# Kernel tuning notes

Hardware: AMD Instinct MI355X
Metric: run time of the kernel (lower is better)

## Reference

```python
import jax, jax.numpy as jnp
import numpy as np

K, D, N = 32, 64, 65536
LOG_2PI = float(np.log(2.0 * np.pi))


def setup_inputs() -> dict:
    key = jax.random.key(0)
    k1, k2, k3, k4 = jax.random.split(key, 4)
    X = jax.random.normal(k1, (N, D), dtype=jnp.float32)
    loc = jax.random.normal(k2, (K, D), dtype=jnp.float32)
    # SPD full covariances per component: A A^T + I
    A = 0.1 * jax.random.normal(k3, (K, D, D), dtype=jnp.float32)
    cov = jnp.einsum('kij,klj->kil', A, A) + jnp.eye(D, dtype=jnp.float32)
    pi = jax.random.normal(k4, (K,), dtype=jnp.float32)
    return {"X": X, "loc": loc, "cov": cov, "pi": pi}


def _gmm_log_prob(X, loc, cov, pi):
    d = X.shape[-1]
    L = jnp.linalg.cholesky(cov)                       # [K, d, d]
    diff = X[:, None, :] - loc[None, :, :]             # [N, K, d]
    # per-component triangular solve: z_k = L_k^{-1} (x - mu_k)
    solve = lambda Lk, dk: jax.scipy.linalg.solve_triangular(Lk, dk.T, lower=True)  # [d, N]
    z = jax.vmap(solve, in_axes=(0, 1))(L, diff)       # [K, d, N]
    maha = jnp.sum(z * z, axis=1).T                    # [N, K]
    half_logdet = jnp.sum(jnp.log(jnp.diagonal(L, axis1=-2, axis2=-1)), axis=-1)  # [K]
    comp_logp = -0.5 * (d * LOG_2PI + maha) - half_logdet[None, :]  # [N, K]
    # Categorical(softmax(pi)).logits followed by log_softmax == log_softmax(pi)
    weighted = comp_logp + jax.nn.log_softmax(pi)[None, :]
    return jax.scipy.special.logsumexp(weighted, axis=1, keepdims=True)  # [N, 1]


def reference(X, loc, cov, pi):
    return _gmm_log_prob(X, loc, cov, pi)
```

## Files before the change

kernel.cpp:

```cpp
#include <hip/hip_runtime.h>
#include <math.h>

#define KCOMP 32
#define DDIM 64
#define LOG_2PI 1.8378770664093453f

#define WFRAG_HALF8S 64
#define WCOMP_BYTES 10240

typedef _Float16 half8 __attribute__((ext_vector_type(8)));
typedef float floatx16 __attribute__((ext_vector_type(16)));

__device__ inline float rdlane(float v, int l) {
    return __uint_as_float(__builtin_amdgcn_readlane(__float_as_uint(v), l));
}

template <int J>
__device__ __forceinline__ void fused_step(float (&Srow)[DDIM], float (&Lrow)[DDIM],
                                           float (&Mcol)[DDIM], float& mydiag,
                                           const int t) {
    constexpr int NPAD = ((J + 7) / 8) * 8;
    float a[8] = {0.f, 0.f, 0.f, 0.f, 0.f, 0.f, 0.f, 0.f};
    float m[8] = {0.f, 0.f, 0.f, 0.f, 0.f, 0.f, 0.f, 0.f};
    #pragma unroll
    for (int p8 = 0; p8 < NPAD; p8 += 8) {
        float b[8];
        #pragma unroll
        for (int e = 0; e < 8; ++e) b[e] = rdlane(Lrow[p8 + e], J);
        #pragma unroll
        for (int e = 0; e < 8; ++e) {
            a[e] += Lrow[p8 + e] * b[e];
            m[e] += b[e] * Mcol[p8 + e];
        }
    }
    float dot = ((a[0] + a[1]) + (a[2] + a[3])) + ((a[4] + a[5]) + (a[6] + a[7]));
    float ms  = ((m[0] + m[1]) + (m[2] + m[3])) + ((m[4] + m[5]) + (m[6] + m[7]));
    float v  = Srow[J] - dot;
    float dj = rdlane(v, J);
    float r  = rsqrtf(dj);
    r = r * (1.5f - 0.5f * dj * r * r);
    Lrow[J] = (t >= J) ? v * r : 0.f;
    Mcol[J] = (t < J) ? (-ms * r) : ((t == J) ? r : 0.f);
    if (t == J) mydiag = dj;
}

template <int J>
__device__ __forceinline__ void fused_run(float (&Srow)[DDIM], float (&Lrow)[DDIM],
                                          float (&Mcol)[DDIM], float& mydiag,
                                          const int t) {
    fused_step<J>(Srow, Lrow, Mcol, mydiag, t);
    if constexpr (J + 1 < DDIM) fused_run<J + 1>(Srow, Lrow, Mcol, mydiag, t);
}

__global__ __launch_bounds__(256, 1) void gmm_prep(const float* __restrict__ loc,
                                                   const float* __restrict__ cov,
                                                   const float* __restrict__ pi,
                                                   _Float16* __restrict__ wt,
                                                   float* __restrict__ cstout)
{
    const int wave = threadIdx.x >> 6;
    const int t    = threadIdx.x & 63;
    const int k    = blockIdx.x * 4 + wave;

    __shared__ float M[4][DDIM][DDIM + 1];
    __shared__ float mu_s[4][DDIM];

    float Srow[DDIM];
    float Lrow[DDIM];
    float Mcol[DDIM];

    {
        const float4* Sg = (const float4*)(cov + (size_t)k * DDIM * DDIM + (size_t)t * DDIM);
        #pragma unroll
        for (int q = 0; q < DDIM / 4; ++q) {
            float4 v = Sg[q];
            Srow[q * 4 + 0] = v.x; Srow[q * 4 + 1] = v.y;
            Srow[q * 4 + 2] = v.z; Srow[q * 4 + 3] = v.w;
        }
    }
    #pragma unroll
    for (int i = 0; i < DDIM; ++i) { Lrow[i] = 0.f; Mcol[i] = 0.f; }
    mu_s[wave][t] = loc[k * DDIM + t];

    float mydiag = 1.f;
    fused_run<0>(Srow, Lrow, Mcol, mydiag, t);

    float hld;
    {
        float lg = 0.5f * logf(mydiag);
        #pragma unroll
        for (int w = 1; w < 64; w <<= 1) lg += __shfl_xor(lg, w);
        hld = lg;
    }

    #pragma unroll
    for (int i = 0; i < DDIM; ++i) M[wave][i][t] = Mcol[i];

    float bt = 0.f;
    #pragma unroll 4
    for (int j = 0; j < DDIM; ++j) bt += M[wave][t][j] * mu_s[wave][j];

    {
        const int r = t >> 5, lrow = t & 31;
        half8* wp = (half8*)wt;
        const size_t fbase = ((size_t)k * 2 + r) * 5;
        #pragma unroll
        for (int c = 0; c < 8; ++c) {
            half8 v;
            #pragma unroll
            for (int e = 0; e < 8; ++e) v[e] = (_Float16)M[wave][t][c * 8 + e];
            int fl = lrow + 32 * (c & 1);
            wp[(fbase + (c >> 1)) * WFRAG_HALF8S + fl] = v;
        }
        {
            float nb = -bt;
            _Float16 h0 = (_Float16)nb;
            _Float16 h1 = (_Float16)(nb - (float)h0);
            half8 v;
            #pragma unroll
            for (int e = 0; e < 8; ++e) v[e] = (_Float16)0.f;
            v[0] = h0; v[1] = h1;
            wp[(fbase + 4) * WFRAG_HALF8S + lrow] = v;
        }
        {
            half8 v;
            #pragma unroll
            for (int e = 0; e < 8; ++e) v[e] = (_Float16)0.f;
            wp[(fbase + 4) * WFRAG_HALF8S + lrow + 32] = v;
        }
    }

    if (t == 0) {
        float mxp = pi[0];
        for (int i = 1; i < KCOMP; ++i) mxp = fmaxf(mxp, pi[i]);
        float s = 0.f;
        for (int i = 0; i < KCOMP; ++i) s += __expf(pi[i] - mxp);
        float lse = mxp + logf(s);
        cstout[k] = (pi[k] - lse) - hld - 0.5f * (float)DDIM * LOG_2PI;
    }
}

__global__ __launch_bounds__(256, 1) void gmm_main(const float* __restrict__ X,
                                                   const _Float16* __restrict__ wt,
                                                   const float* __restrict__ cst,
                                                   float* __restrict__ out)
{
    __shared__ float2 part[4][128];

    const int tid  = threadIdx.x;
    const int wave = tid >> 6;
    const int lane = tid & 63;
    const int col  = lane & 31;
    const int h    = lane >> 5;
    const int ptbase = blockIdx.x * 128;

    half8 bf[4][5];
    #pragma unroll
    for (int g = 0; g < 4; ++g) {
        const float* xr = X + (size_t)(ptbase + g * 32 + col) * DDIM;
        #pragma unroll
        for (int s = 0; s < 4; ++s) {
            int c = s * 2 + h;
            float4 lo = *(const float4*)(xr + c * 8);
            float4 hi = *(const float4*)(xr + c * 8 + 4);
            half8 v;
            v[0] = (_Float16)lo.x; v[1] = (_Float16)lo.y;
            v[2] = (_Float16)lo.z; v[3] = (_Float16)lo.w;
            v[4] = (_Float16)hi.x; v[5] = (_Float16)hi.y;
            v[6] = (_Float16)hi.z; v[7] = (_Float16)hi.w;
            bf[g][s] = v;
        }
        half8 v;
        #pragma unroll
        for (int e = 0; e < 8; ++e) v[e] = (_Float16)0.f;
        if (h == 0) { v[0] = (_Float16)1.f; v[1] = (_Float16)1.f; }
        bf[g][4] = v;
    }

    const half8* wp = (const half8*)wt;
    const int comp0 = wave * 8;

    float mx[4], sm[4];
    #pragma unroll
    for (int g = 0; g < 4; ++g) { mx[g] = -INFINITY; sm[g] = 0.f; }

    half8 wfA[5], wfB[5];
    #pragma unroll
    for (int s = 0; s < 5; ++s)
        wfA[s] = wp[((size_t)comp0 * 2 + 0) * 5 * WFRAG_HALF8S + s * WFRAG_HALF8S + lane];

    #pragma unroll 1
    for (int q = 0; q < 8; ++q) {
        const int c = comp0 + q;

        #pragma unroll
        for (int s = 0; s < 5; ++s)
            wfB[s] = wp[((size_t)c * 2 + 1) * 5 * WFRAG_HALF8S + s * WFRAG_HALF8S + lane];

        float sP[4];

        {
            floatx16 a0 = {0.f}, a1 = {0.f}, a2 = {0.f}, a3 = {0.f};
            #pragma unroll
            for (int s = 0; s < 5; ++s) {
                a0 = __builtin_amdgcn_mfma_f32_32x32x16_f16(wfA[s], bf[0][s], a0, 0, 0, 0);
                a1 = __builtin_amdgcn_mfma_f32_32x32x16_f16(wfA[s], bf[1][s], a1, 0, 0, 0);
                a2 = __builtin_amdgcn_mfma_f32_32x32x16_f16(wfA[s], bf[2][s], a2, 0, 0, 0);
                a3 = __builtin_amdgcn_mfma_f32_32x32x16_f16(wfA[s], bf[3][s], a3, 0, 0, 0);
            }
            float p0 = 0.f, p1 = 0.f, p2 = 0.f, p3 = 0.f;
            #pragma unroll
            for (int r = 0; r < 16; ++r) {
                p0 += a0[r] * a0[r]; p1 += a1[r] * a1[r];
                p2 += a2[r] * a2[r]; p3 += a3[r] * a3[r];
            }
            sP[0] = p0; sP[1] = p1; sP[2] = p2; sP[3] = p3;
        }

        if (q < 7) {
            #pragma unroll
            for (int s = 0; s < 5; ++s)
                wfA[s] = wp[((size_t)(c + 1) * 2 + 0) * 5 * WFRAG_HALF8S + s * WFRAG_HALF8S + lane];
        }

        {
            floatx16 a0 = {0.f}, a1 = {0.f}, a2 = {0.f}, a3 = {0.f};
            #pragma unroll
            for (int s = 0; s < 5; ++s) {
                a0 = __builtin_amdgcn_mfma_f32_32x32x16_f16(wfB[s], bf[0][s], a0, 0, 0, 0);
                a1 = __builtin_amdgcn_mfma_f32_32x32x16_f16(wfB[s], bf[1][s], a1, 0, 0, 0);
                a2 = __builtin_amdgcn_mfma_f32_32x32x16_f16(wfB[s], bf[2][s], a2, 0, 0, 0);
                a3 = __builtin_amdgcn_mfma_f32_32x32x16_f16(wfB[s], bf[3][s], a3, 0, 0, 0);
            }
            float p0 = 0.f, p1 = 0.f, p2 = 0.f, p3 = 0.f;
            #pragma unroll
            for (int r = 0; r < 16; ++r) {
                p0 += a0[r] * a0[r]; p1 += a1[r] * a1[r];
                p2 += a2[r] * a2[r]; p3 += a3[r] * a3[r];
            }
            sP[0] += p0; sP[1] += p1; sP[2] += p2; sP[3] += p3;
        }

        const float ck = cst[c];
        #pragma unroll
        for (int g = 0; g < 4; ++g) {
            float sfull = sP[g] + __shfl_xor(sP[g], 32);
            float lp = ck - 0.5f * sfull;
            float nm = fmaxf(mx[g], lp);
            sm[g] = sm[g] * __expf(mx[g] - nm) + __expf(lp - nm);
            mx[g] = nm;
        }
    }

    if (h == 0) {
        #pragma unroll
        for (int g = 0; g < 4; ++g)
            part[wave][g * 32 + col] = make_float2(mx[g], sm[g]);
    }
    __syncthreads();

    if (tid < 128) {
        float2 p0 = part[0][tid], p1 = part[1][tid];
        float2 p2 = part[2][tid], p3 = part[3][tid];
        float m = fmaxf(fmaxf(p0.x, p1.x), fmaxf(p2.x, p3.x));
        float s = p0.y * __expf(p0.x - m) + p1.y * __expf(p1.x - m)
                + p2.y * __expf(p2.x - m) + p3.y * __expf(p3.x - m);
        out[ptbase + tid] = m + logf(s);
    }
}

extern "C" void kernel_launch(void* const* d_in, const int* in_sizes, int n_in,
                              void* d_out, int out_size, void* d_ws, size_t ws_size,
                              hipStream_t stream) {
    const float* X   = (const float*)d_in[0];
    const float* loc = (const float*)d_in[1];
    const float* cov = (const float*)d_in[2];
    const float* pi  = (const float*)d_in[3];
    float* out = (float*)d_out;

    char* ws = (char*)d_ws;
    _Float16* wt = (_Float16*)ws;
    float* cstp  = (float*)(ws + (size_t)KCOMP * WCOMP_BYTES);

    const int n = in_sizes[0] / DDIM;

    gmm_prep<<<KCOMP / 4, 256, 0, stream>>>(loc, cov, pi, wt, cstp);
    gmm_main<<<n / 128, 256, 0, stream>>>(X, wt, cstp, out);
}
```

Baseline: 52.46 us.

## Move Cholesky factor state from registers to LDS with rolled loops

After: 103.4 us. 1.97x slower.

```diff
diff --git a/kernel.cpp b/kernel.cpp
--- a/kernel.cpp
+++ b/kernel.cpp
@@ -13,43 +13,6 @@
 
 __device__ inline float rdlane(float v, int l) {
     return __uint_as_float(__builtin_amdgcn_readlane(__float_as_uint(v), l));
-}
-
-template <int J>
-__device__ __forceinline__ void fused_step(float (&Srow)[DDIM], float (&Lrow)[DDIM],
-                                           float (&Mcol)[DDIM], float& mydiag,
-                                           const int t) {
-    constexpr int NPAD = ((J + 7) / 8) * 8;
-    float a[8] = {0.f, 0.f, 0.f, 0.f, 0.f, 0.f, 0.f, 0.f};
-    float m[8] = {0.f, 0.f, 0.f, 0.f, 0.f, 0.f, 0.f, 0.f};
-    #pragma unroll
-    for (int p8 = 0; p8 < NPAD; p8 += 8) {
-        float b[8];
-        #pragma unroll
-        for (int e = 0; e < 8; ++e) b[e] = rdlane(Lrow[p8 + e], J);
-        #pragma unroll
-        for (int e = 0; e < 8; ++e) {
-            a[e] += Lrow[p8 + e] * b[e];
-            m[e] += b[e] * Mcol[p8 + e];
-        }
-    }
-    float dot = ((a[0] + a[1]) + (a[2] + a[3])) + ((a[4] + a[5]) + (a[6] + a[7]));
-    float ms  = ((m[0] + m[1]) + (m[2] + m[3])) + ((m[4] + m[5]) + (m[6] + m[7]));
-    float v  = Srow[J] - dot;
-    float dj = rdlane(v, J);
-    float r  = rsqrtf(dj);
-    r = r * (1.5f - 0.5f * dj * r * r);
-    Lrow[J] = (t >= J) ? v * r : 0.f;
-    Mcol[J] = (t < J) ? (-ms * r) : ((t == J) ? r : 0.f);
-    if (t == J) mydiag = dj;
-}
-
-template <int J>
-__device__ __forceinline__ void fused_run(float (&Srow)[DDIM], float (&Lrow)[DDIM],
-                                          float (&Mcol)[DDIM], float& mydiag,
-                                          const int t) {
-    fused_step<J>(Srow, Lrow, Mcol, mydiag, t);
-    if constexpr (J + 1 < DDIM) fused_run<J + 1>(Srow, Lrow, Mcol, mydiag, t);
 }
 
 __global__ __launch_bounds__(256, 1) void gmm_prep(const float* __restrict__ loc,
@@ -62,28 +25,57 @@
     const int t    = threadIdx.x & 63;
     const int k    = blockIdx.x * 4 + wave;
 
-    __shared__ float M[4][DDIM][DDIM + 1];
+    __shared__ float Ls[4][DDIM][DDIM + 1];
+    __shared__ float Ms[4][DDIM][DDIM + 1];
     __shared__ float mu_s[4][DDIM];
 
-    float Srow[DDIM];
-    float Lrow[DDIM];
-    float Mcol[DDIM];
-
-    {
-        const float4* Sg = (const float4*)(cov + (size_t)k * DDIM * DDIM + (size_t)t * DDIM);
-        #pragma unroll
-        for (int q = 0; q < DDIM / 4; ++q) {
-            float4 v = Sg[q];
-            Srow[q * 4 + 0] = v.x; Srow[q * 4 + 1] = v.y;
-            Srow[q * 4 + 2] = v.z; Srow[q * 4 + 3] = v.w;
-        }
-    }
-    #pragma unroll
-    for (int i = 0; i < DDIM; ++i) { Lrow[i] = 0.f; Mcol[i] = 0.f; }
+    float (*Lw)[DDIM + 1] = Ls[wave];
+    float (*Mw)[DDIM + 1] = Ms[wave];
+
+    const float* sg = cov + (size_t)k * DDIM * DDIM + (size_t)t * DDIM;
     mu_s[wave][t] = loc[k * DDIM + t];
 
+    const float* Lt = &Lw[t][0];
+    const float* Mt = &Mw[0][t];
+
     float mydiag = 1.f;
-    fused_run<0>(Srow, Lrow, Mcol, mydiag, t);
+    float scur = sg[0];
+
+    #pragma unroll 1
+    for (int j = 0; j < DDIM; ++j) {
+        float snext = sg[(j + 1 < DDIM) ? (j + 1) : (DDIM - 1)];
+
+        const float* Lj = &Lw[j][0];
+        float a0 = 0.f, a1 = 0.f, a2 = 0.f, a3 = 0.f;
+        float m0 = 0.f, m1 = 0.f, m2 = 0.f, m3 = 0.f;
+        int c = 0;
+        #pragma unroll 1
+        for (; c + 4 <= j; c += 4) {
+            float b0 = Lj[c], b1 = Lj[c + 1], b2 = Lj[c + 2], b3 = Lj[c + 3];
+            float l0 = Lt[c], l1 = Lt[c + 1], l2 = Lt[c + 2], l3 = Lt[c + 3];
+            float q0 = Mt[c * (DDIM + 1)],       q1 = Mt[(c + 1) * (DDIM + 1)];
+            float q2 = Mt[(c + 2) * (DDIM + 1)], q3 = Mt[(c + 3) * (DDIM + 1)];
+            a0 += l0 * b0; a1 += l1 * b1; a2 += l2 * b2; a3 += l3 * b3;
+            m0 += b0 * q0; m1 += b1 * q1; m2 += b2 * q2; m3 += b3 * q3;
+        }
+        #pragma unroll 1
+        for (; c < j; ++c) {
+            float b0 = Lj[c];
+            a0 += Lt[c] * b0;
+            m0 += b0 * Mt[c * (DDIM + 1)];
+        }
+        float dot = (a0 + a1) + (a2 + a3);
+        float ms  = (m0 + m1) + (m2 + m3);
+
+        float v  = scur - dot;
+        float dj = rdlane(v, j);
+        float r  = rsqrtf(dj);
+        r = r * (1.5f - 0.5f * dj * r * r);
+        Lw[t][j] = (t >= j) ? v * r : 0.f;
+        Mw[j][t] = (t < j) ? (-ms * r) : ((t == j) ? r : 0.f);
+        if (t == j) mydiag = dj;
+        scur = snext;
+    }
 
     float hld;
     {
@@ -93,12 +85,9 @@
         hld = lg;
     }
 
-    #pragma unroll
-    for (int i = 0; i < DDIM; ++i) M[wave][i][t] = Mcol[i];
-
     float bt = 0.f;
     #pragma unroll 4
-    for (int j = 0; j < DDIM; ++j) bt += M[wave][t][j] * mu_s[wave][j];
+    for (int q = 0; q < DDIM; ++q) bt += Mw[t][q] * mu_s[wave][q];
 
     {
         const int r = t >> 5, lrow = t & 31;
@@ -108,7 +97,7 @@
         for (int c = 0; c < 8; ++c) {
             half8 v;
             #pragma unroll
-            for (int e = 0; e < 8; ++e) v[e] = (_Float16)M[wave][t][c * 8 + e];
+            for (int e = 0; e < 8; ++e) v[e] = (_Float16)Mw[t][c * 8 + e];
             int fl = lrow + 32 * (c & 1);
             wp[(fbase + (c >> 1)) * WFRAG_HALF8S + fl] = v;
         }
```
